# Kernel optimization log

Measured on AMD Instinct MI355X. Metric: run time of the kernel, lower is better.

Reference implementation:

```python
import jax, jax.numpy as jnp
import numpy as np

N_NODES = 50000
N_EDGES = 500000
D = 128
OUT = 1


def setup_inputs() -> dict:
    key = jax.random.key(0)
    k_h, k_e, k_s, k_d, k_w = jax.random.split(key, 5)
    h = jax.random.normal(k_h, (N_NODES, D), dtype=jnp.float32)
    e = jax.random.normal(k_e, (N_EDGES, D), dtype=jnp.float32)
    src = jax.random.randint(k_s, (N_EDGES,), 0, N_NODES, dtype=jnp.int64)
    dst = jax.random.randint(k_d, (N_EDGES,), 0, N_NODES, dtype=jnp.int64)
    W = jax.random.normal(k_w, (OUT, 3 * D), dtype=jnp.float32) * (1.0 / np.sqrt(3 * D))
    b = jnp.zeros((OUT,), dtype=jnp.float32)
    return {"h": h, "e": e, "src": src, "dst": dst, "W": W, "b": b}


def reference(h, e, src, dst, W, b):
    # Gather per-edge source/destination node features, concat with edge feats.
    h_k = h[src]                      # [E, D]
    h_i = h[dst]                      # [E, D]
    # Avoid materializing the [E, 3D] concat: split the weight and sum GEMVs.
    Wk, Wi, We = W[:, :D], W[:, D:2 * D], W[:, 2 * D:]   # each [OUT, D]
    logits = (h_k @ Wk.T) + (h_i @ Wi.T) + (e @ We.T) + b  # [E, OUT]
    return jax.nn.sigmoid(logits)
```

## Files before the change

### kernel.cpp

```cpp
#include <hip/hip_runtime.h>
#include <math.h>

#define DIM 128

typedef float vfloat4 __attribute__((ext_vector_type(4)));
typedef int   vint4   __attribute__((ext_vector_type(4)));

__device__ __forceinline__ float reduce16(float v) {
    v += __shfl_xor(v, 1);
    v += __shfl_xor(v, 2);
    v += __shfl_xor(v, 4);
    v += __shfl_xor(v, 8);
    return v;
}

__device__ __forceinline__ float dp4(vfloat4 a, vfloat4 b) {
    return a.x * b.x + a.y * b.y + a.z * b.z + a.w * b.w;
}

__device__ __forceinline__ vfloat4 ntload(const float* p) {
    return __builtin_nontemporal_load(reinterpret_cast<const vfloat4*>(p));
}

__global__ __launch_bounds__(256) void node_proj_kernel(
        const float* __restrict__ h,
        const float* __restrict__ W,
        float* __restrict__ pk,
        float* __restrict__ pi,
        int n_nodes) {
    const int l = threadIdx.x & 15;
    const int group0 = (blockIdx.x * blockDim.x + threadIdx.x) >> 4;
    const int ngroups = (gridDim.x * blockDim.x) >> 4;

    const vfloat4 wk0 = *reinterpret_cast<const vfloat4*>(W + 4 * l);
    const vfloat4 wk1 = *reinterpret_cast<const vfloat4*>(W + 64 + 4 * l);
    const vfloat4 wi0 = *reinterpret_cast<const vfloat4*>(W + DIM + 4 * l);
    const vfloat4 wi1 = *reinterpret_cast<const vfloat4*>(W + DIM + 64 + 4 * l);

    const int n_full = n_nodes & ~3;

    for (int base = 4 * group0; base < n_full; base += 4 * ngroups) {
        const float* hp = h + (size_t)base * DIM;
        vfloat4 a0[4], a1[4];
#pragma unroll
        for (int j = 0; j < 4; ++j) {
            a0[j] = ntload(hp + (size_t)j * DIM + 4 * l);
            a1[j] = ntload(hp + (size_t)j * DIM + 64 + 4 * l);
        }
        float sk[4], si[4];
#pragma unroll
        for (int j = 0; j < 4; ++j) {
            sk[j] = reduce16(dp4(a0[j], wk0) + dp4(a1[j], wk1));
            si[j] = reduce16(dp4(a0[j], wi0) + dp4(a1[j], wi1));
        }
        if (l == 0) {
            vfloat4 vk; vk.x = sk[0]; vk.y = sk[1]; vk.z = sk[2]; vk.w = sk[3];
            vfloat4 vi; vi.x = si[0]; vi.y = si[1]; vi.z = si[2]; vi.w = si[3];
            *reinterpret_cast<vfloat4*>(pk + base) = vk;
            *reinterpret_cast<vfloat4*>(pi + base) = vi;
        }
    }
    for (int node = n_full + group0; node < n_nodes; node += ngroups) {
        const float* hp = h + (size_t)node * DIM;
        const vfloat4 a0 = ntload(hp + 4 * l);
        const vfloat4 a1 = ntload(hp + 64 + 4 * l);
        float sk = reduce16(dp4(a0, wk0) + dp4(a1, wk1));
        float si = reduce16(dp4(a0, wi0) + dp4(a1, wi1));
        if (l == 0) { pk[node] = sk; pi[node] = si; }
    }
}

__global__ __launch_bounds__(256) void edge_kernel(
        const float* __restrict__ e,
        const int* __restrict__ src,
        const int* __restrict__ dst,
        const float* __restrict__ W,
        const float* __restrict__ b,
        const float* __restrict__ pk,
        const float* __restrict__ pi,
        float* __restrict__ out,
        int n_edges) {
    const int l = threadIdx.x & 15;
    const int group0 = (blockIdx.x * blockDim.x + threadIdx.x) >> 4;
    const int ngroups = (gridDim.x * blockDim.x) >> 4;

    const vfloat4 we0 = *reinterpret_cast<const vfloat4*>(W + 2 * DIM + 4 * l);
    const vfloat4 we1 = *reinterpret_cast<const vfloat4*>(W + 2 * DIM + 64 + 4 * l);
    const float b0 = b[0];

    const int n_full = n_edges & ~3;

    for (int base = 4 * group0; base < n_full; base += 4 * ngroups) {
        const vint4 s4 = *reinterpret_cast<const vint4*>(src + base);
        const vint4 d4 = *reinterpret_cast<const vint4*>(dst + base);
        float pkv[4], piv[4];
        pkv[0] = pk[s4.x]; pkv[1] = pk[s4.y]; pkv[2] = pk[s4.z]; pkv[3] = pk[s4.w];
        piv[0] = pi[d4.x]; piv[1] = pi[d4.y]; piv[2] = pi[d4.z]; piv[3] = pi[d4.w];

        const float* ep = e + (size_t)base * DIM;
        vfloat4 a0[4], a1[4];
#pragma unroll
        for (int j = 0; j < 4; ++j) {
            a0[j] = ntload(ep + (size_t)j * DIM + 4 * l);
            a1[j] = ntload(ep + (size_t)j * DIM + 64 + 4 * l);
        }

        float s[4];
#pragma unroll
        for (int j = 0; j < 4; ++j)
            s[j] = reduce16(dp4(a0[j], we0) + dp4(a1[j], we1));

        if (l == 0) {
            vfloat4 o;
            o.x = 1.0f / (1.0f + __expf(-(s[0] + pkv[0] + piv[0] + b0)));
            o.y = 1.0f / (1.0f + __expf(-(s[1] + pkv[1] + piv[1] + b0)));
            o.z = 1.0f / (1.0f + __expf(-(s[2] + pkv[2] + piv[2] + b0)));
            o.w = 1.0f / (1.0f + __expf(-(s[3] + pkv[3] + piv[3] + b0)));
            *reinterpret_cast<vfloat4*>(out + base) = o;
        }
    }
    for (int edge = n_full + group0; edge < n_edges; edge += ngroups) {
        const int si_ = src[edge];
        const int di_ = dst[edge];
        const float pkv = pk[si_];
        const float piv = pi[di_];
        const float* ep = e + (size_t)edge * DIM;
        const vfloat4 a0 = ntload(ep + 4 * l);
        const vfloat4 a1 = ntload(ep + 64 + 4 * l);
        float s = reduce16(dp4(a0, we0) + dp4(a1, we1));
        if (l == 0) {
            out[edge] = 1.0f / (1.0f + __expf(-(s + pkv + piv + b0)));
        }
    }
}

__global__ void edge_fused_kernel(const float* __restrict__ h,
                                  const float* __restrict__ e,
                                  const int* __restrict__ src,
                                  const int* __restrict__ dst,
                                  const float* __restrict__ W,
                                  const float* __restrict__ b,
                                  float* __restrict__ out,
                                  int n_edges) {
    int tid  = blockIdx.x * blockDim.x + threadIdx.x;
    int edge = tid >> 5;
    int l    = tid & 31;
    if (edge >= n_edges) return;

    int s_idx = src[edge];
    int d_idx = dst[edge];

    const float4 hk = *reinterpret_cast<const float4*>(h + (size_t)s_idx * DIM + 4 * l);
    const float4 hi = *reinterpret_cast<const float4*>(h + (size_t)d_idx * DIM + 4 * l);
    const float4 ev = *reinterpret_cast<const float4*>(e + (size_t)edge * DIM + 4 * l);
    const float4 wk = *reinterpret_cast<const float4*>(W + 4 * l);
    const float4 wi = *reinterpret_cast<const float4*>(W + DIM + 4 * l);
    const float4 we = *reinterpret_cast<const float4*>(W + 2 * DIM + 4 * l);

    float s = hk.x * wk.x + hk.y * wk.y + hk.z * wk.z + hk.w * wk.w
            + hi.x * wi.x + hi.y * wi.y + hi.z * wi.z + hi.w * wi.w
            + ev.x * we.x + ev.y * we.y + ev.z * we.z + ev.w * we.w;
    s += __shfl_xor(s, 1);
    s += __shfl_xor(s, 2);
    s += __shfl_xor(s, 4);
    s += __shfl_xor(s, 8);
    s += __shfl_xor(s, 16);

    if (l == 0) {
        float logit = s + b[0];
        out[edge] = 1.0f / (1.0f + expf(-logit));
    }
}

extern "C" void kernel_launch(void* const* d_in, const int* in_sizes, int n_in,
                              void* d_out, int out_size, void* d_ws, size_t ws_size,
                              hipStream_t stream) {
    const float* h   = (const float*)d_in[0];
    const float* e   = (const float*)d_in[1];
    const int*   src = (const int*)d_in[2];
    const int*   dst = (const int*)d_in[3];
    const float* W   = (const float*)d_in[4];
    const float* b   = (const float*)d_in[5];
    float* out = (float*)d_out;

    const int n_nodes = in_sizes[0] / DIM;
    const int n_edges = in_sizes[2];

    const size_t ws_needed = 2 * (size_t)n_nodes * sizeof(float);

    if (ws_size >= ws_needed) {
        float* pk = (float*)d_ws;
        float* pi = pk + n_nodes;

        {
            const int block = 256;
            long total = ((long)n_nodes + 3) / 4 * 16;
            int grid = (int)((total + block - 1) / block);
            if (grid > 2048) grid = 2048;
            node_proj_kernel<<<grid, block, 0, stream>>>(h, W, pk, pi, n_nodes);
        }
        {
            const int block = 256;
            long total = ((long)n_edges + 3) / 4 * 16;
            int grid = (int)((total + block - 1) / block);
            if (grid > 2048) grid = 2048;
            edge_kernel<<<grid, block, 0, stream>>>(e, src, dst, W, b, pk, pi, out, n_edges);
        }
    } else {
        int total = n_edges * 32;
        int block = 256;
        int grid  = (total + block - 1) / block;
        edge_fused_kernel<<<grid, block, 0, stream>>>(h, e, src, dst, W, b, out, n_edges);
    }
}
```

Measured before the change: 50.79 us.

## Run node and edge projections concurrently in one kernel, then gather-finish pass

Combines the node projection and the edge-feature GEMV into a single launch, with the first 200 blocks handling nodes and the rest handling edges. This removes the serial dependency so the large edge stream no longer waits on the node pass. The edge partial sums go to a workspace buffer, and a light finish kernel gathers pk/pi, adds the bias and applies the sigmoid. The cost is an extra launch plus writing and reading an edge-sized intermediate. The fallback two-kernel path is simplified to one item per group.

```diff
diff --git a/kernel.cpp b/kernel.cpp
--- a/kernel.cpp
+++ b/kernel.cpp
@@ -20,6 +20,132 @@
 
 __device__ __forceinline__ vfloat4 ntload(const float* p) {
     return __builtin_nontemporal_load(reinterpret_cast<const vfloat4*>(p));
+}
+
+__device__ __forceinline__ float sigmoidf(float x) {
+    return 1.0f / (1.0f + __expf(-x));
+}
+
+__global__ __launch_bounds__(256) void fused_A(
+        const float* __restrict__ h,
+        const float* __restrict__ e,
+        const float* __restrict__ W,
+        float* __restrict__ pk,
+        float* __restrict__ pi,
+        float* __restrict__ s_e,
+        int n_nodes,
+        int n_edges,
+        int node_blocks) {
+    const int l = threadIdx.x & 15;
+
+    if ((int)blockIdx.x < node_blocks) {
+        const int group0 = ((blockIdx.x << 8) + threadIdx.x) >> 4;
+        const int ngroups = node_blocks << 4;
+
+        const vfloat4 wk0 = *reinterpret_cast<const vfloat4*>(W + 4 * l);
+        const vfloat4 wk1 = *reinterpret_cast<const vfloat4*>(W + 64 + 4 * l);
+        const vfloat4 wi0 = *reinterpret_cast<const vfloat4*>(W + DIM + 4 * l);
+        const vfloat4 wi1 = *reinterpret_cast<const vfloat4*>(W + DIM + 64 + 4 * l);
+
+        const int n_full = n_nodes & ~3;
+
+        for (int base = 4 * group0; base < n_full; base += 4 * ngroups) {
+            const float* hp = h + (size_t)base * DIM;
+            vfloat4 a0[4], a1[4];
+#pragma unroll
+            for (int j = 0; j < 4; ++j) {
+                a0[j] = ntload(hp + (size_t)j * DIM + 4 * l);
+                a1[j] = ntload(hp + (size_t)j * DIM + 64 + 4 * l);
+            }
+            float sk[4], si[4];
+#pragma unroll
+            for (int j = 0; j < 4; ++j) {
+                sk[j] = reduce16(dp4(a0[j], wk0) + dp4(a1[j], wk1));
+                si[j] = reduce16(dp4(a0[j], wi0) + dp4(a1[j], wi1));
+            }
+            if (l == 0) {
+                vfloat4 vk; vk.x = sk[0]; vk.y = sk[1]; vk.z = sk[2]; vk.w = sk[3];
+                vfloat4 vi; vi.x = si[0]; vi.y = si[1]; vi.z = si[2]; vi.w = si[3];
+                *reinterpret_cast<vfloat4*>(pk + base) = vk;
+                *reinterpret_cast<vfloat4*>(pi + base) = vi;
+            }
+        }
+        for (int node = n_full + group0; node < n_nodes; node += ngroups) {
+            const float* hp = h + (size_t)node * DIM;
+            const vfloat4 a0 = ntload(hp + 4 * l);
+            const vfloat4 a1 = ntload(hp + 64 + 4 * l);
+            float sk = reduce16(dp4(a0, wk0) + dp4(a1, wk1));
+            float si = reduce16(dp4(a0, wi0) + dp4(a1, wi1));
+            if (l == 0) { pk[node] = sk; pi[node] = si; }
+        }
+    } else {
+        const int bid2 = (int)blockIdx.x - node_blocks;
+        const int group0 = ((bid2 << 8) + threadIdx.x) >> 4;
+        const int ngroups = ((int)gridDim.x - node_blocks) << 4;
+
+        const vfloat4 we0 = *reinterpret_cast<const vfloat4*>(W + 2 * DIM + 4 * l);
+        const vfloat4 we1 = *reinterpret_cast<const vfloat4*>(W + 2 * DIM + 64 + 4 * l);
+
+        const int n_full = n_edges & ~3;
+
+        for (int base = 4 * group0; base < n_full; base += 4 * ngroups) {
+            const float* ep = e + (size_t)base * DIM;
+            vfloat4 a0[4], a1[4];
+#pragma unroll
+            for (int j = 0; j < 4; ++j) {
+                a0[j] = ntload(ep + (size_t)j * DIM + 4 * l);
+                a1[j] = ntload(ep + (size_t)j * DIM + 64 + 4 * l);
+            }
+            float s[4];
+#pragma unroll
+            for (int j = 0; j < 4; ++j)
+                s[j] = reduce16(dp4(a0[j], we0) + dp4(a1[j], we1));
+
+            if (l == 0) {
+                vfloat4 o; o.x = s[0]; o.y = s[1]; o.z = s[2]; o.w = s[3];
+                *reinterpret_cast<vfloat4*>(s_e + base) = o;
+            }
+        }
+        for (int edge = n_full + group0; edge < n_edges; edge += ngroups) {
+            const float* ep = e + (size_t)edge * DIM;
+            const vfloat4 a0 = ntload(ep + 4 * l);
+            const vfloat4 a1 = ntload(ep + 64 + 4 * l);
+            float s = reduce16(dp4(a0, we0) + dp4(a1, we1));
+            if (l == 0) s_e[edge] = s;
+        }
+    }
+}
+
+__global__ __launch_bounds__(256) void finish_kernel(
+        const int* __restrict__ src,
+        const int* __restrict__ dst,
+        const float* __restrict__ b,
+        const float* __restrict__ pk,
+        const float* __restrict__ pi,
+        const float* __restrict__ s_e,
+        float* __restrict__ out,
+        int n_edges) {
+    const int tid = blockIdx.x * blockDim.x + threadIdx.x;
+    const int nthreads = gridDim.x * blockDim.x;
+    const int n_full = n_edges & ~3;
+    const float b0 = b[0];
+
+    for (int base = 4 * tid; base < n_full; base += 4 * nthreads) {
+        const vint4 s4 = *reinterpret_cast<const vint4*>(src + base);
+        const vint4 d4 = *reinterpret_cast<const vint4*>(dst + base);
+        const vfloat4 se = *reinterpret_cast<const vfloat4*>(s_e + base);
+        const float pk0 = pk[s4.x], pk1 = pk[s4.y], pk2 = pk[s4.z], pk3 = pk[s4.w];
+        const float pi0 = pi[d4.x], pi1 = pi[d4.y], pi2 = pi[d4.z], pi3 = pi[d4.w];
+        vfloat4 o;
+        o.x = sigmoidf(se.x + pk0 + pi0 + b0);
+        o.y = sigmoidf(se.y + pk1 + pi1 + b0);
+        o.z = sigmoidf(se.z + pk2 + pi2 + b0);
+        o.w = sigmoidf(se.w + pk3 + pi3 + b0);
+        *reinterpret_cast<vfloat4*>(out + base) = o;
+    }
+    for (int edge = n_full + tid; edge < n_edges; edge += nthreads) {
+        out[edge] = sigmoidf(s_e[edge] + pk[src[edge]] + pi[dst[edge]] + b0);
+    }
 }
 
 __global__ __launch_bounds__(256) void node_proj_kernel(
@@ -37,30 +163,7 @@
     const vfloat4 wi0 = *reinterpret_cast<const vfloat4*>(W + DIM + 4 * l);
     const vfloat4 wi1 = *reinterpret_cast<const vfloat4*>(W + DIM + 64 + 4 * l);
 
-    const int n_full = n_nodes & ~3;
-
-    for (int base = 4 * group0; base < n_full; base += 4 * ngroups) {
-        const float* hp = h + (size_t)base * DIM;
-        vfloat4 a0[4], a1[4];
-#pragma unroll
-        for (int j = 0; j < 4; ++j) {
-            a0[j] = ntload(hp + (size_t)j * DIM + 4 * l);
-            a1[j] = ntload(hp + (size_t)j * DIM + 64 + 4 * l);
-        }
-        float sk[4], si[4];
-#pragma unroll
-        for (int j = 0; j < 4; ++j) {
-            sk[j] = reduce16(dp4(a0[j], wk0) + dp4(a1[j], wk1));
-            si[j] = reduce16(dp4(a0[j], wi0) + dp4(a1[j], wi1));
-        }
-        if (l == 0) {
-            vfloat4 vk; vk.x = sk[0]; vk.y = sk[1]; vk.z = sk[2]; vk.w = sk[3];
-            vfloat4 vi; vi.x = si[0]; vi.y = si[1]; vi.z = si[2]; vi.w = si[3];
-            *reinterpret_cast<vfloat4*>(pk + base) = vk;
-            *reinterpret_cast<vfloat4*>(pi + base) = vi;
-        }
-    }
-    for (int node = n_full + group0; node < n_nodes; node += ngroups) {
+    for (int node = group0; node < n_nodes; node += ngroups) {
         const float* hp = h + (size_t)node * DIM;
         const vfloat4 a0 = ntload(hp + 4 * l);
         const vfloat4 a1 = ntload(hp + 64 + 4 * l);
@@ -88,48 +191,17 @@
     const vfloat4 we1 = *reinterpret_cast<const vfloat4*>(W + 2 * DIM + 64 + 4 * l);
     const float b0 = b[0];
 
-    const int n_full = n_edges & ~3;
-
-    for (int base = 4 * group0; base < n_full; base += 4 * ngroups) {
-        const vint4 s4 = *reinterpret_cast<const vint4*>(src + base);
-        const vint4 d4 = *reinterpret_cast<const vint4*>(dst + base);
-        float pkv[4], piv[4];
-        pkv[0] = pk[s4.x]; pkv[1] = pk[s4.y]; pkv[2] = pk[s4.z]; pkv[3] = pk[s4.w];
-        piv[0] = pi[d4.x]; piv[1] = pi[d4.y]; piv[2] = pi[d4.z]; piv[3] = pi[d4.w];
-
-        const float* ep = e + (size_t)base * DIM;
-        vfloat4 a0[4], a1[4];
-#pragma unroll
-        for (int j = 0; j < 4; ++j) {
-            a0[j] = ntload(ep + (size_t)j * DIM + 4 * l);
-            a1[j] = ntload(ep + (size_t)j * DIM + 64 + 4 * l);
-        }
-
-        float s[4];
-#pragma unroll
-        for (int j = 0; j < 4; ++j)
-            s[j] = reduce16(dp4(a0[j], we0) + dp4(a1[j], we1));
-
-        if (l == 0) {
-            vfloat4 o;
-            o.x = 1.0f / (1.0f + __expf(-(s[0] + pkv[0] + piv[0] + b0)));
-            o.y = 1.0f / (1.0f + __expf(-(s[1] + pkv[1] + piv[1] + b0)));
-            o.z = 1.0f / (1.0f + __expf(-(s[2] + pkv[2] + piv[2] + b0)));
-            o.w = 1.0f / (1.0f + __expf(-(s[3] + pkv[3] + piv[3] + b0)));
-            *reinterpret_cast<vfloat4*>(out + base) = o;
-        }
-    }
-    for (int edge = n_full + group0; edge < n_edges; edge += ngroups) {
-        const int si_ = src[edge];
-        const int di_ = dst[edge];
-        const float pkv = pk[si_];
-        const float piv = pi[di_];
+    for (int edge = group0; edge < n_edges; edge += ngroups) {
+        const int s_idx = src[edge];
+        const int d_idx = dst[edge];
+        const float pkv = pk[s_idx];
+        const float piv = pi[d_idx];
         const float* ep = e + (size_t)edge * DIM;
         const vfloat4 a0 = ntload(ep + 4 * l);
         const vfloat4 a1 = ntload(ep + 64 + 4 * l);
         float s = reduce16(dp4(a0, we0) + dp4(a1, we1));
         if (l == 0) {
-            out[edge] = 1.0f / (1.0f + __expf(-(s + pkv + piv + b0)));
+            out[edge] = sigmoidf(s + pkv + piv + b0);
         }
     }
 }
@@ -186,22 +258,39 @@
     const int n_nodes = in_sizes[0] / DIM;
     const int n_edges = in_sizes[2];
 
-    const size_t ws_needed = 2 * (size_t)n_nodes * sizeof(float);
-
-    if (ws_size >= ws_needed) {
+    const int n_nodes_pad = (n_nodes + 3) & ~3;
+    const size_t ws_full = ((size_t)2 * n_nodes_pad + (size_t)n_edges) * sizeof(float);
+    const size_t ws_mid  = (size_t)2 * n_nodes_pad * sizeof(float);
+
+    if (ws_size >= ws_full) {
+        float* pk  = (float*)d_ws;
+        float* pi  = pk + n_nodes_pad;
+        float* s_e = pi + n_nodes_pad;
+
+        const int grid_a = 2048;
+        const int node_blocks = 200;
+        fused_A<<<grid_a, 256, 0, stream>>>(h, e, W, pk, pi, s_e,
+                                            n_nodes, n_edges, node_blocks);
+
+        long threads_b = ((long)n_edges + 3) / 4;
+        int grid_b = (int)((threads_b + 255) / 256);
+        if (grid_b > 2048) grid_b = 2048;
+        if (grid_b < 1) grid_b = 1;
+        finish_kernel<<<grid_b, 256, 0, stream>>>(src, dst, b, pk, pi, s_e, out, n_edges);
+    } else if (ws_size >= ws_mid) {
         float* pk = (float*)d_ws;
-        float* pi = pk + n_nodes;
+        float* pi = pk + n_nodes_pad;
 
         {
             const int block = 256;
-            long total = ((long)n_nodes + 3) / 4 * 16;
+            long total = (long)n_nodes * 16;
             int grid = (int)((total + block - 1) / block);
             if (grid > 2048) grid = 2048;
             node_proj_kernel<<<grid, block, 0, stream>>>(h, W, pk, pi, n_nodes);
         }
         {
             const int block = 256;
-            long total = ((long)n_edges + 3) / 4 * 16;
+            long total = (long)n_edges * 16;
             int grid = (int)((total + block - 1) / block);
             if (grid > 2048) grid = 2048;
             edge_kernel<<<grid, block, 0, stream>>>(e, src, dst, W, b, pk, pi, out, n_edges);
```

Measured after the change: 55.51 us. +9.3%, slower.

## Fuse node projection and edge pass into one persistent kernel with grid sync

Applied to the files above, without the earlier changes.

Replaces the two-kernel sequence with a single persistent kernel of 2048 blocks. Blocks first claim node chunks through an atomic counter to compute the per-node projections, then compute their edge-feature dot products into LDS. They then spin on a release/acquire completion counter before gathering the node projections and writing the sigmoid outputs. The aim is to remove the second launch and the gap between kernels, and to overlap the edge streaming with the node phase. The cost is an extra memset, a spin-wait that assumes all 2048 blocks are co-resident, and a bounded spin that could break early and read incomplete data.

```diff
diff --git a/kernel.cpp b/kernel.cpp
--- a/kernel.cpp
+++ b/kernel.cpp
@@ -2,6 +2,9 @@
 #include <math.h>
 
 #define DIM 128
+#define NODE_CHUNK 64
+#define QPB_MAX 64
+#define GRID_P 2048
 
 typedef float vfloat4 __attribute__((ext_vector_type(4)));
 typedef int   vint4   __attribute__((ext_vector_type(4)));
@@ -20,6 +23,143 @@
 
 __device__ __forceinline__ vfloat4 ntload(const float* p) {
     return __builtin_nontemporal_load(reinterpret_cast<const vfloat4*>(p));
+}
+
+__device__ __forceinline__ float sigmoidf(float x) {
+    return 1.0f / (1.0f + __expf(-x));
+}
+
+__global__ __launch_bounds__(256) void fused_persistent(
+        const float* __restrict__ h,
+        const float* __restrict__ e,
+        const int* __restrict__ src,
+        const int* __restrict__ dst,
+        const float* __restrict__ W,
+        const float* __restrict__ b,
+        int* __restrict__ ctrs,
+        float* __restrict__ pk,
+        float* __restrict__ pi,
+        float* __restrict__ out,
+        int n_nodes, int n_edges, int nchunks, int qpb) {
+    __shared__ float s_lds[QPB_MAX * 4];
+    __shared__ int   lsrc[QPB_MAX * 4];
+    __shared__ int   ldst[QPB_MAX * 4];
+    __shared__ int   c_bcast;
+
+    const int tid = threadIdx.x;
+    const int l   = tid & 15;
+    const int g   = tid >> 4;
+
+    {
+        const vfloat4 wk0 = *reinterpret_cast<const vfloat4*>(W + 4 * l);
+        const vfloat4 wk1 = *reinterpret_cast<const vfloat4*>(W + 64 + 4 * l);
+        const vfloat4 wi0 = *reinterpret_cast<const vfloat4*>(W + DIM + 4 * l);
+        const vfloat4 wi1 = *reinterpret_cast<const vfloat4*>(W + DIM + 64 + 4 * l);
+
+        int my_chunks = 0;
+        for (;;) {
+            if (tid == 0) c_bcast = atomicAdd(&ctrs[0], 1);
+            __syncthreads();
+            const int c = c_bcast;
+            __syncthreads();
+            if (c >= nchunks) break;
+            ++my_chunks;
+
+            const int nb = c * NODE_CHUNK + 4 * g;
+            if (nb < n_nodes) {
+                const bool full = (nb + 4 <= n_nodes);
+                vfloat4 a0[4], a1[4];
+#pragma unroll
+                for (int j = 0; j < 4; ++j) {
+                    int row = nb + j;
+                    if (row > n_nodes - 1) row = n_nodes - 1;
+                    const float* hp = h + (size_t)row * DIM;
+                    a0[j] = ntload(hp + 4 * l);
+                    a1[j] = ntload(hp + 64 + 4 * l);
+                }
+                float sk[4], si[4];
+#pragma unroll
+                for (int j = 0; j < 4; ++j) {
+                    sk[j] = reduce16(dp4(a0[j], wk0) + dp4(a1[j], wk1));
+                    si[j] = reduce16(dp4(a0[j], wi0) + dp4(a1[j], wi1));
+                }
+                if (l == 0) {
+                    if (full) {
+                        vfloat4 vk; vk.x = sk[0]; vk.y = sk[1]; vk.z = sk[2]; vk.w = sk[3];
+                        vfloat4 vi; vi.x = si[0]; vi.y = si[1]; vi.z = si[2]; vi.w = si[3];
+                        *reinterpret_cast<vfloat4*>(pk + nb) = vk;
+                        *reinterpret_cast<vfloat4*>(pi + nb) = vi;
+                    } else {
+                        for (int j = 0; j < 4 && nb + j < n_nodes; ++j) {
+                            pk[nb + j] = sk[j];
+                            pi[nb + j] = si[j];
+                        }
+                    }
+                }
+            }
+        }
+        __syncthreads();
+        if (tid == 0 && my_chunks > 0) {
+            __hip_atomic_fetch_add(&ctrs[1], my_chunks,
+                                   __ATOMIC_RELEASE, __HIP_MEMORY_SCOPE_AGENT);
+        }
+    }
+
+    const int NQ = (n_edges + 3) >> 2;
+    const int q0 = (int)blockIdx.x * qpb;
+    const int q1 = min(q0 + qpb, NQ);
+    const int e0 = q0 * 4;
+    const int e_end = min(q1 * 4, n_edges);
+    const int edges_blk = e_end - e0;
+
+    for (int t = tid; t < edges_blk; t += 256) {
+        lsrc[t] = src[e0 + t];
+        ldst[t] = dst[e0 + t];
+    }
+
+    {
+        const vfloat4 we0 = *reinterpret_cast<const vfloat4*>(W + 2 * DIM + 4 * l);
+        const vfloat4 we1 = *reinterpret_cast<const vfloat4*>(W + 2 * DIM + 64 + 4 * l);
+
+        for (int qq = q0 + g; qq < q1; qq += 16) {
+            const int base = qq * 4;
+            vfloat4 a0[4], a1[4];
+#pragma unroll
+            for (int j = 0; j < 4; ++j) {
+                int row = base + j;
+                if (row > n_edges - 1) row = n_edges - 1;
+                const float* ep = e + (size_t)row * DIM;
+                a0[j] = ntload(ep + 4 * l);
+                a1[j] = ntload(ep + 64 + 4 * l);
+            }
+            float s[4];
+#pragma unroll
+            for (int j = 0; j < 4; ++j)
+                s[j] = reduce16(dp4(a0[j], we0) + dp4(a1[j], we1));
+            if (l == 0) {
+                vfloat4 o; o.x = s[0]; o.y = s[1]; o.z = s[2]; o.w = s[3];
+                *reinterpret_cast<vfloat4*>(&s_lds[(qq - q0) * 4]) = o;
+            }
+        }
+    }
+
+    if (tid == 0) {
+        long spins = 0;
+        while (__hip_atomic_load(&ctrs[1], __ATOMIC_ACQUIRE,
+                                 __HIP_MEMORY_SCOPE_AGENT) < nchunks) {
+            __builtin_amdgcn_s_sleep(8);
+            if (++spins > (1L << 28)) break;
+        }
+    }
+    __syncthreads();
+
+    if (tid < edges_blk) {
+        const float b0  = b[0];
+        const float sv  = s_lds[tid];
+        const float pkv = pk[lsrc[tid]];
+        const float piv = pi[ldst[tid]];
+        out[e0 + tid] = sigmoidf(sv + pkv + piv + b0);
+    }
 }
 
 __global__ __launch_bounds__(256) void node_proj_kernel(
@@ -37,30 +177,7 @@
     const vfloat4 wi0 = *reinterpret_cast<const vfloat4*>(W + DIM + 4 * l);
     const vfloat4 wi1 = *reinterpret_cast<const vfloat4*>(W + DIM + 64 + 4 * l);
 
-    const int n_full = n_nodes & ~3;
-
-    for (int base = 4 * group0; base < n_full; base += 4 * ngroups) {
-        const float* hp = h + (size_t)base * DIM;
-        vfloat4 a0[4], a1[4];
-#pragma unroll
-        for (int j = 0; j < 4; ++j) {
-            a0[j] = ntload(hp + (size_t)j * DIM + 4 * l);
-            a1[j] = ntload(hp + (size_t)j * DIM + 64 + 4 * l);
-        }
-        float sk[4], si[4];
-#pragma unroll
-        for (int j = 0; j < 4; ++j) {
-            sk[j] = reduce16(dp4(a0[j], wk0) + dp4(a1[j], wk1));
-            si[j] = reduce16(dp4(a0[j], wi0) + dp4(a1[j], wi1));
-        }
-        if (l == 0) {
-            vfloat4 vk; vk.x = sk[0]; vk.y = sk[1]; vk.z = sk[2]; vk.w = sk[3];
-            vfloat4 vi; vi.x = si[0]; vi.y = si[1]; vi.z = si[2]; vi.w = si[3];
-            *reinterpret_cast<vfloat4*>(pk + base) = vk;
-            *reinterpret_cast<vfloat4*>(pi + base) = vi;
-        }
-    }
-    for (int node = n_full + group0; node < n_nodes; node += ngroups) {
+    for (int node = group0; node < n_nodes; node += ngroups) {
         const float* hp = h + (size_t)node * DIM;
         const vfloat4 a0 = ntload(hp + 4 * l);
         const vfloat4 a1 = ntload(hp + 64 + 4 * l);
@@ -104,7 +221,6 @@
             a0[j] = ntload(ep + (size_t)j * DIM + 4 * l);
             a1[j] = ntload(ep + (size_t)j * DIM + 64 + 4 * l);
         }
-
         float s[4];
 #pragma unroll
         for (int j = 0; j < 4; ++j)
@@ -112,25 +228,21 @@
 
         if (l == 0) {
             vfloat4 o;
-            o.x = 1.0f / (1.0f + __expf(-(s[0] + pkv[0] + piv[0] + b0)));
-            o.y = 1.0f / (1.0f + __expf(-(s[1] + pkv[1] + piv[1] + b0)));
-            o.z = 1.0f / (1.0f + __expf(-(s[2] + pkv[2] + piv[2] + b0)));
-            o.w = 1.0f / (1.0f + __expf(-(s[3] + pkv[3] + piv[3] + b0)));
+            o.x = sigmoidf(s[0] + pkv[0] + piv[0] + b0);
+            o.y = sigmoidf(s[1] + pkv[1] + piv[1] + b0);
+            o.z = sigmoidf(s[2] + pkv[2] + piv[2] + b0);
+            o.w = sigmoidf(s[3] + pkv[3] + piv[3] + b0);
             *reinterpret_cast<vfloat4*>(out + base) = o;
         }
     }
     for (int edge = n_full + group0; edge < n_edges; edge += ngroups) {
-        const int si_ = src[edge];
-        const int di_ = dst[edge];
-        const float pkv = pk[si_];
-        const float piv = pi[di_];
+        const float pkv = pk[src[edge]];
+        const float piv = pi[dst[edge]];
         const float* ep = e + (size_t)edge * DIM;
         const vfloat4 a0 = ntload(ep + 4 * l);
         const vfloat4 a1 = ntload(ep + 64 + 4 * l);
         float s = reduce16(dp4(a0, we0) + dp4(a1, we1));
-        if (l == 0) {
-            out[edge] = 1.0f / (1.0f + __expf(-(s + pkv + piv + b0)));
-        }
+        if (l == 0) out[edge] = sigmoidf(s + pkv + piv + b0);
     }
 }
 
@@ -186,15 +298,31 @@
     const int n_nodes = in_sizes[0] / DIM;
     const int n_edges = in_sizes[2];
 
-    const size_t ws_needed = 2 * (size_t)n_nodes * sizeof(float);
-
-    if (ws_size >= ws_needed) {
+    const int n_nodes_pad = (n_nodes + 3) & ~3;
+    const size_t ws_persist = 16 + (size_t)2 * n_nodes_pad * sizeof(float);
+    const size_t ws_mid     = (size_t)2 * n_nodes_pad * sizeof(float);
+
+    const int NQ  = (n_edges + 3) / 4;
+    const int qpb = (NQ + GRID_P - 1) / GRID_P;
+
+    if (ws_size >= ws_persist && qpb <= QPB_MAX) {
+        int*   ctrs = (int*)d_ws;
+        float* pk   = (float*)((char*)d_ws + 16);
+        float* pi   = pk + n_nodes_pad;
+
+        hipMemsetAsync(d_ws, 0, 16, stream);
+
+        const int nchunks = (n_nodes + NODE_CHUNK - 1) / NODE_CHUNK;
+        fused_persistent<<<GRID_P, 256, 0, stream>>>(
+            h, e, src, dst, W, b, ctrs, pk, pi, out,
+            n_nodes, n_edges, nchunks, qpb);
+    } else if (ws_size >= ws_mid) {
         float* pk = (float*)d_ws;
-        float* pi = pk + n_nodes;
+        float* pi = pk + n_nodes_pad;
 
         {
             const int block = 256;
-            long total = ((long)n_nodes + 3) / 4 * 16;
+            long total = (long)n_nodes * 16;
             int grid = (int)((total + block - 1) / block);
             if (grid > 2048) grid = 2048;
             node_proj_kernel<<<grid, block, 0, stream>>>(h, W, pk, pi, n_nodes);
```

New measurement: 139.4 us. 2.74x slower.
